# Optimization experiments

Measured on AMD Instinct MI355X. Metric: run time of the kernel, lower is better.

Reference implementation:

```python
import jax, jax.numpy as jnp
import numpy as np

EMBED_DIM = 1024
HEADS = 16
HEAD_DIM = EMBED_DIM // HEADS
DIST_LAMBDA = -0.1
LN_EPS = 1e-5


def setup_inputs() -> dict:
    key = jax.random.key(0)
    ks = jax.random.split(key, 16)
    B, N, D = 32, 4096, EMBED_DIM
    s = 1.0 / np.sqrt(D)
    inp = {
        "query": jax.random.normal(ks[0], (B, D), jnp.float32),
        "context": jax.random.normal(ks[1], (B, N, D), jnp.float32),
        "dist_matrix": jax.random.uniform(ks[2], (B, 1, N), jnp.float32),
        "context_mask": jax.random.randint(ks[3], (B, N), 0, 2, jnp.int32),
        "Wq": jax.random.normal(ks[4], (D, D), jnp.float32) * s,
        "bq": jnp.zeros((D,), jnp.float32),
        "Wk": jax.random.normal(ks[5], (D, D), jnp.float32) * s,
        "bk": jnp.zeros((D,), jnp.float32),
        "Wv": jax.random.normal(ks[6], (D, D), jnp.float32) * s,
        "bv": jnp.zeros((D,), jnp.float32),
        "Wo": jax.random.normal(ks[7], (D, D), jnp.float32) * s,
        "bo": jnp.zeros((D,), jnp.float32),
        "ln_gamma": jnp.ones((D,), jnp.float32),
        "ln_beta": jnp.zeros((D,), jnp.float32),
    }
    return inp


def reference(query, context, dist_matrix, context_mask,
              Wq, bq, Wk, bk, Wv, bv, Wo, bo, ln_gamma, ln_beta):
    B, N, D = context.shape
    H, hd = HEADS, HEAD_DIM
    # projections
    q = (query @ Wq + bq).reshape(B, H, hd)            # [B,H,hd] (single query)
    k = (context @ Wk + bk).reshape(B, N, H, hd)       # [B,N,H,hd]
    v = (context @ Wv + bv).reshape(B, N, H, hd)
    # scores: [B,H,N]
    scores = jnp.einsum("bhd,bnhd->bhn", q, k) / np.sqrt(hd)
    # additive Manhattan-distance bias, broadcast over heads
    scores = scores + dist_matrix * DIST_LAMBDA        # dist_matrix [B,1,N]
    # mask
    scores = jnp.where(context_mask[:, None, :] == 0, -1e9, scores)
    attn = jax.nn.softmax(scores, axis=-1)             # [B,H,N]
    attn_out = jnp.einsum("bhn,bnhd->bhd", attn, v).reshape(B, D)
    output = attn_out @ Wo + bo
    x = query + output
    # LayerNorm
    mu = jnp.mean(x, axis=-1, keepdims=True)
    var = jnp.mean((x - mu) ** 2, axis=-1, keepdims=True)
    return (x - mu) * jax.lax.rsqrt(var + LN_EPS) * ln_gamma + ln_beta
```

## Files before the change

### kernel.cpp

```cpp
#include <hip/hip_runtime.h>
#include <hip/hip_bf16.h>
#include <math.h>

#define DDIM 1024
#define NH 16
#define HDIM 64
#define SCALE 0.125f
#define DLAM -0.1f
#define LNEPS 1e-5f
#define NS 16
#define CHW 16
#define BROW 256
#define CBSTR 1032

typedef short bf16x8 __attribute__((ext_vector_type(8)));
typedef float f32x4 __attribute__((ext_vector_type(4)));

__device__ inline unsigned short f2bf(float x) {
    return __builtin_bit_cast(unsigned short, __float2bfloat16(x));
}
__device__ inline float bfhi2f(unsigned u) {
    return __builtin_bit_cast(float, u & 0xffff0000u);
}
__device__ inline float bflo2f(unsigned u) {
    return __builtin_bit_cast(float, u << 16);
}

__global__ __launch_bounds__(512) void k_q(const float* __restrict__ query,
                                           const float* __restrict__ Wq,
                                           const float* __restrict__ bq,
                                           float* __restrict__ qout) {
    int b = blockIdx.x, c0 = blockIdx.y * 128;
    __shared__ float qs[DDIM];
    __shared__ float ps[512];
    int t = threadIdx.x;
    for (int i = t; i < DDIM; i += 512) qs[i] = query[b * DDIM + i];
    __syncthreads();
    int cl = t & 127;
    int col = c0 + cl;
    int d0 = (t >> 7) * 256;
    float acc = 0.f;
#pragma unroll 8
    for (int d = d0; d < d0 + 256; ++d)
        acc = fmaf(qs[d], Wq[(size_t)d * DDIM + col], acc);
    ps[t] = acc;
    __syncthreads();
    if (t < 128)
        qout[b * DDIM + col] = ps[t] + ps[t + 128] + ps[t + 256] + ps[t + 384] + bq[col];
}

__global__ __launch_bounds__(256) void k_qp(const float* __restrict__ qin,
                                            const float* __restrict__ Wk,
                                            unsigned short* __restrict__ qpb) {
    int b = blockIdx.x, dt = blockIdx.y;
    __shared__ float qs[DDIM];
    for (int i = threadIdx.x; i < DDIM; i += 256) qs[i] = qin[b * DDIM + i];
    __syncthreads();
    int h = threadIdx.x & 15, dl = threadIdx.x >> 4;
    int d = dt * 16 + dl;
    const float* wr = Wk + (size_t)d * DDIM + h * HDIM;
    const float* qh = qs + h * HDIM;
    float acc = 0.f;
#pragma unroll
    for (int j = 0; j < HDIM; ++j) acc = fmaf(wr[j], qh[j], acc);
    qpb[((size_t)(b * NH + h)) * DDIM + d] = f2bf(acc * SCALE);
}

__global__ __launch_bounds__(512) void k_sb(const float* __restrict__ qin,
                                            const float* __restrict__ bk,
                                            float* __restrict__ sb) {
    int idx = threadIdx.x;
    int b = idx >> 4, h = idx & 15;
    float acc = 0.f;
#pragma unroll
    for (int j = 0; j < HDIM; ++j)
        acc = fmaf(bk[h * HDIM + j], qin[b * DDIM + h * HDIM + j], acc);
    sb[idx] = acc * SCALE;
}

__global__ __launch_bounds__(256, 2) void k_flash2(
    const float* __restrict__ ctx, const unsigned short* __restrict__ qpb,
    const float* __restrict__ sb, const float* __restrict__ dist,
    const int* __restrict__ mask, float* __restrict__ partA,
    float* __restrict__ partM, float* __restrict__ partL, int N) {
    __shared__ unsigned short cbuf[2][CHW][CBSTR];
    __shared__ float red[4][CHW][17];
    __shared__ float P_lds[CHW][20];
    __shared__ float fh_lds[NH];
    __shared__ float dls[BROW];

    int b = blockIdx.x, ns = blockIdx.y;
    int t = threadIdx.x, lane = t & 63, w = t >> 6;
    int m = lane & 15, g = lane >> 4;
    int nb0 = ns * BROW;
    int NIT = BROW / CHW;

    {
        float dv = dist[(size_t)b * N + nb0 + t] * DLAM;
        dls[t] = mask[(size_t)b * N + nb0 + t] ? dv : -1e30f;
    }
    bf16x8 qf[8];
#pragma unroll
    for (int j = 0; j < 8; ++j)
        qf[j] = *reinterpret_cast<const bf16x8*>(
            qpb + ((size_t)(b * NH + m)) * DDIM + w * 256 + j * 32 + g * 8);
    float sbv = sb[b * NH + m];

    f32x4 acc[NH];
#pragma unroll
    for (int h = 0; h < NH; ++h) acc[h] = (f32x4){0.f, 0.f, 0.f, 0.f};
    float m_run = -1e30f, l_run = 0.f;

    const float4* cb4 = reinterpret_cast<const float4*>(ctx) +
                        ((size_t)b * N + nb0) * (DDIM / 4);
    float4 inflight[16];

#define LOADC(c)                                               \
    {                                                          \
        const float4* src = cb4 + (size_t)(c) * CHW * (DDIM / 4); \
        _Pragma("unroll") for (int i = 0; i < 16; ++i)         \
            inflight[i] = src[i * 256 + t];                    \
    }
#define WRITECB(buf)                                                        \
    {                                                                       \
        _Pragma("unroll") for (int i = 0; i < 16; ++i) {                    \
            float4 v = inflight[i];                                         \
            unsigned lo = (unsigned)f2bf(v.x) | ((unsigned)f2bf(v.y) << 16);\
            unsigned hi = (unsigned)f2bf(v.z) | ((unsigned)f2bf(v.w) << 16);\
            *reinterpret_cast<uint2*>(&cbuf[buf][i][t * 4]) =               \
                make_uint2(lo, hi);                                         \
        }                                                                   \
    }

    LOADC(0);
    WRITECB(0);
    LOADC(1);

    for (int c = 0; c < NIT; ++c) {
        __syncthreads();
        int buf = c & 1;
        f32x4 cS = {0.f, 0.f, 0.f, 0.f};
#pragma unroll
        for (int j = 0; j < 8; ++j) {
            bf16x8 a = *reinterpret_cast<const bf16x8*>(
                &cbuf[buf][m][w * 256 + j * 32 + g * 8]);
            cS = __builtin_amdgcn_mfma_f32_16x16x32_bf16(a, qf[j], cS, 0, 0, 0);
        }
#pragma unroll
        for (int r = 0; r < 4; ++r) red[w][g * 4 + r][m] = cS[r];
        __syncthreads();
        float S[4];
#pragma unroll
        for (int r = 0; r < 4; ++r) {
            int n = g * 4 + r;
            S[r] = red[0][n][m] + red[1][n][m] + red[2][n][m] + red[3][n][m] +
                   sbv + dls[c * CHW + n];
        }
        float cm = fmaxf(fmaxf(S[0], S[1]), fmaxf(S[2], S[3]));
        cm = fmaxf(cm, __shfl_xor(cm, 16, 64));
        cm = fmaxf(cm, __shfl_xor(cm, 32, 64));
        float mnew = fmaxf(m_run, cm);
        float f = __expf(m_run - mnew);
        float p[4];
        float ls = 0.f;
#pragma unroll
        for (int r = 0; r < 4; ++r) {
            p[r] = __expf(S[r] - mnew);
            ls += p[r];
        }
        ls += __shfl_xor(ls, 16, 64);
        ls += __shfl_xor(ls, 32, 64);
        l_run = l_run * f + ls;
        m_run = mnew;
#pragma unroll
        for (int r = 0; r < 4; ++r) P_lds[g * 4 + r][m] = p[r];
        if (w == 0 && g == 0) fh_lds[m] = f;
        __syncthreads();
#pragma unroll
        for (int h = 0; h < NH; ++h) acc[h] *= fh_lds[h];
        int dq = w * 256 + lane * 4;
#pragma unroll 4
        for (int n = 0; n < CHW; ++n) {
            uint2 cw = *reinterpret_cast<const uint2*>(&cbuf[buf][n][dq]);
            float cv0 = bflo2f(cw.x), cv1 = bfhi2f(cw.x);
            float cv2 = bflo2f(cw.y), cv3 = bfhi2f(cw.y);
            float4 P0 = *reinterpret_cast<const float4*>(&P_lds[n][0]);
            float4 P1 = *reinterpret_cast<const float4*>(&P_lds[n][4]);
            float4 P2 = *reinterpret_cast<const float4*>(&P_lds[n][8]);
            float4 P3 = *reinterpret_cast<const float4*>(&P_lds[n][12]);
            float Pv[16] = {P0.x, P0.y, P0.z, P0.w, P1.x, P1.y, P1.z, P1.w,
                            P2.x, P2.y, P2.z, P2.w, P3.x, P3.y, P3.z, P3.w};
#pragma unroll
            for (int h = 0; h < NH; ++h) {
                acc[h][0] = fmaf(Pv[h], cv0, acc[h][0]);
                acc[h][1] = fmaf(Pv[h], cv1, acc[h][1]);
                acc[h][2] = fmaf(Pv[h], cv2, acc[h][2]);
                acc[h][3] = fmaf(Pv[h], cv3, acc[h][3]);
            }
        }
        __syncthreads();
        if (c + 1 < NIT) {
            WRITECB(buf ^ 1);
            if (c + 2 < NIT) LOADC(c + 2);
        }
    }

    int dq = w * 256 + lane * 4;
#pragma unroll
    for (int h = 0; h < NH; ++h) {
        float4 o = make_float4(acc[h][0], acc[h][1], acc[h][2], acc[h][3]);
        *reinterpret_cast<float4*>(
            partA + ((size_t)((b * NS + ns) * NH + h)) * DDIM + dq) = o;
    }
    if (t < NH) {
        partM[(b * NS + ns) * NH + t] = m_run;
        partL[(b * NS + ns) * NH + t] = l_run;
    }
#undef LOADC
#undef WRITECB
}

__global__ __launch_bounds__(256) void k_comb(const float* __restrict__ partA,
                                              const float* __restrict__ partM,
                                              const float* __restrict__ partL,
                                              float* __restrict__ ctxa) {
    int row = blockIdx.x;
    int b = row >> 4, h = row & 15;
    float M = -1e30f;
#pragma unroll
    for (int ns = 0; ns < NS; ++ns)
        M = fmaxf(M, partM[(b * NS + ns) * NH + h]);
    float denom = 0.f;
#pragma unroll
    for (int ns = 0; ns < NS; ++ns)
        denom = fmaf(__expf(partM[(b * NS + ns) * NH + h] - M),
                     partL[(b * NS + ns) * NH + h], denom);
    float inv = 1.f / denom;
    int d4 = threadIdx.x * 4;
    float4 a = make_float4(0.f, 0.f, 0.f, 0.f);
#pragma unroll 8
    for (int ns = 0; ns < NS; ++ns) {
        float wv = __expf(partM[(b * NS + ns) * NH + h] - M);
        float4 v = *reinterpret_cast<const float4*>(
            partA + ((size_t)((b * NS + ns) * NH + h)) * DDIM + d4);
        a.x = fmaf(wv, v.x, a.x);
        a.y = fmaf(wv, v.y, a.y);
        a.z = fmaf(wv, v.z, a.z);
        a.w = fmaf(wv, v.w, a.w);
    }
    float4 o = make_float4(a.x * inv, a.y * inv, a.z * inv, a.w * inv);
    *reinterpret_cast<float4*>(ctxa + (size_t)row * DDIM + d4) = o;
}

__global__ __launch_bounds__(256) void k_vproj(const float* __restrict__ ctxa,
                                               const float* __restrict__ Wv,
                                               const float* __restrict__ bv,
                                               float* __restrict__ oattn) {
    int b = blockIdx.x, c0 = blockIdx.y * 128;
    int h0 = c0 >> 6;
    __shared__ float cs[2][DDIM];
    __shared__ float ps[256];
    for (int i = threadIdx.x; i < 2 * DDIM; i += 256)
        cs[i >> 10][i & 1023] =
            ctxa[((size_t)(b * NH + h0 + (i >> 10))) * DDIM + (i & 1023)];
    __syncthreads();
    int t = threadIdx.x;
    int cl = t & 127;
    int col = c0 + cl;
    int hl = cl >> 6;
    int d0 = (t >> 7) * 512;
    float acc = 0.f;
#pragma unroll 8
    for (int d = d0; d < d0 + 512; ++d)
        acc = fmaf(cs[hl][d], Wv[(size_t)d * DDIM + col], acc);
    ps[t] = acc;
    __syncthreads();
    if (t < 128) oattn[b * DDIM + col] = ps[t] + ps[t + 128] + bv[col];
}

__global__ __launch_bounds__(256) void k_oproj(const float* __restrict__ query,
                                               const float* __restrict__ oattn,
                                               const float* __restrict__ Wo,
                                               const float* __restrict__ bo,
                                               float* __restrict__ x) {
    int b = blockIdx.x, c0 = blockIdx.y * 128;
    __shared__ float os[DDIM];
    __shared__ float ps[256];
    for (int i = threadIdx.x; i < DDIM; i += 256) os[i] = oattn[b * DDIM + i];
    __syncthreads();
    int t = threadIdx.x;
    int col = c0 + (t & 127);
    int d0 = (t >> 7) * 512;
    float acc = 0.f;
#pragma unroll 8
    for (int d = d0; d < d0 + 512; ++d)
        acc = fmaf(os[d], Wo[(size_t)d * DDIM + col], acc);
    ps[t] = acc;
    __syncthreads();
    if (t < 128)
        x[b * DDIM + col] = query[b * DDIM + col] + ps[t] + ps[t + 128] + bo[col];
}

__global__ __launch_bounds__(256) void k_ln(const float* __restrict__ x,
                                            const float* __restrict__ gamma,
                                            const float* __restrict__ beta,
                                            float* __restrict__ out) {
    int b = blockIdx.x;
    int t = threadIdx.x;
    __shared__ float red[8];
    float xv[4];
    float lsum = 0.f;
#pragma unroll
    for (int k = 0; k < 4; ++k) {
        xv[k] = x[b * DDIM + t + k * 256];
        lsum += xv[k];
    }
#pragma unroll
    for (int off = 32; off > 0; off >>= 1) lsum += __shfl_xor(lsum, off, 64);
    if ((t & 63) == 0) red[t >> 6] = lsum;
    __syncthreads();
    float mu = (red[0] + red[1] + red[2] + red[3]) * (1.f / DDIM);
    float lsq = 0.f;
#pragma unroll
    for (int k = 0; k < 4; ++k) {
        float dx = xv[k] - mu;
        lsq += dx * dx;
    }
#pragma unroll
    for (int off = 32; off > 0; off >>= 1) lsq += __shfl_xor(lsq, off, 64);
    if ((t & 63) == 0) red[4 + (t >> 6)] = lsq;
    __syncthreads();
    float var = (red[4] + red[5] + red[6] + red[7]) * (1.f / DDIM);
    float rstd = rsqrtf(var + LNEPS);
#pragma unroll
    for (int k = 0; k < 4; ++k) {
        int c = t + k * 256;
        out[b * DDIM + c] = (xv[k] - mu) * rstd * gamma[c] + beta[c];
    }
}

extern "C" void kernel_launch(void* const* d_in, const int* in_sizes, int n_in,
                              void* d_out, int out_size, void* d_ws, size_t ws_size,
                              hipStream_t stream) {
    const float* query = (const float*)d_in[0];
    const float* ctx   = (const float*)d_in[1];
    const float* dist  = (const float*)d_in[2];
    const int*   mask  = (const int*)d_in[3];
    const float* Wq = (const float*)d_in[4];
    const float* bq = (const float*)d_in[5];
    const float* Wk = (const float*)d_in[6];
    const float* bk = (const float*)d_in[7];
    const float* Wv = (const float*)d_in[8];
    const float* bv = (const float*)d_in[9];
    const float* Wo = (const float*)d_in[10];
    const float* bo = (const float*)d_in[11];
    const float* gamma = (const float*)d_in[12];
    const float* beta  = (const float*)d_in[13];
    float* out = (float*)d_out;

    int B = in_sizes[0] / DDIM;
    int N = in_sizes[1] / (B * DDIM);

    float* ws = (float*)d_ws;
    float* q = ws;
    unsigned short* qpb = (unsigned short*)(q + (size_t)B * DDIM);
    float* sb = (float*)(qpb + (size_t)B * NH * DDIM);
    float* partA = sb + (size_t)B * NH;
    float* partM = partA + (size_t)B * NS * NH * DDIM;
    float* partL = partM + (size_t)B * NS * NH;
    float* ctxa = partL + (size_t)B * NS * NH;
    float* oattn = ctxa + (size_t)B * NH * DDIM;
    float* xbuf = oattn + (size_t)B * DDIM;

    k_q<<<dim3(B, 8), 512, 0, stream>>>(query, Wq, bq, q);
    k_qp<<<dim3(B, DDIM / 16), 256, 0, stream>>>(q, Wk, qpb);
    k_sb<<<1, B * NH, 0, stream>>>(q, bk, sb);
    k_flash2<<<dim3(B, NS), 256, 0, stream>>>(ctx, qpb, sb, dist, mask,
                                              partA, partM, partL, N);
    k_comb<<<B * NH, 256, 0, stream>>>(partA, partM, partL, ctxa);
    k_vproj<<<dim3(B, 8), 256, 0, stream>>>(ctxa, Wv, bv, oattn);
    k_oproj<<<dim3(B, 8), 256, 0, stream>>>(query, oattn, Wo, bo, xbuf);
    k_ln<<<B, 256, 0, stream>>>(xbuf, gamma, beta, out);
}
```

Measured before the change: 244.7 us.

## Widen flash kernel to 512 threads, single LDS buffer, batch k_qp over 8 queries

The flash-attention stage now runs 512 threads per block across 8 waves. Each wave handles 128 of the feature dimensions with 4 MFMAs, and each thread holds 2 output columns instead of 4, which cuts registers so 4 blocks can target each CU. The double-buffered LDS context tile becomes a single buffer to save LDS, at the cost of serialising the LDS write of the next chunk behind compute. Separately, k_qp now processes 8 batch rows per block so each Wk row is reused across 8 queries instead of being re-read per batch.

```diff
diff --git a/kernel.cpp b/kernel.cpp
--- a/kernel.cpp
+++ b/kernel.cpp
@@ -52,18 +52,26 @@
 __global__ __launch_bounds__(256) void k_qp(const float* __restrict__ qin,
                                             const float* __restrict__ Wk,
                                             unsigned short* __restrict__ qpb) {
-    int b = blockIdx.x, dt = blockIdx.y;
-    __shared__ float qs[DDIM];
-    for (int i = threadIdx.x; i < DDIM; i += 256) qs[i] = qin[b * DDIM + i];
+    int dt = blockIdx.x, bg = blockIdx.y;
+    __shared__ float qs[8][DDIM];
+    for (int i = threadIdx.x; i < 8 * DDIM; i += 256)
+        qs[i >> 10][i & 1023] =
+            qin[(size_t)(bg * 8 + (i >> 10)) * DDIM + (i & 1023)];
     __syncthreads();
     int h = threadIdx.x & 15, dl = threadIdx.x >> 4;
     int d = dt * 16 + dl;
     const float* wr = Wk + (size_t)d * DDIM + h * HDIM;
-    const float* qh = qs + h * HDIM;
-    float acc = 0.f;
-#pragma unroll
-    for (int j = 0; j < HDIM; ++j) acc = fmaf(wr[j], qh[j], acc);
-    qpb[((size_t)(b * NH + h)) * DDIM + d] = f2bf(acc * SCALE);
+    float acc[8] = {0.f, 0.f, 0.f, 0.f, 0.f, 0.f, 0.f, 0.f};
+#pragma unroll
+    for (int j = 0; j < HDIM; ++j) {
+        float wv = wr[j];
+#pragma unroll
+        for (int bb = 0; bb < 8; ++bb)
+            acc[bb] = fmaf(wv, qs[bb][h * HDIM + j], acc[bb]);
+    }
+#pragma unroll
+    for (int bb = 0; bb < 8; ++bb)
+        qpb[((size_t)((bg * 8 + bb) * NH + h)) * DDIM + d] = f2bf(acc[bb] * SCALE);
 }
 
 __global__ __launch_bounds__(512) void k_sb(const float* __restrict__ qin,
@@ -78,13 +86,13 @@
     sb[idx] = acc * SCALE;
 }
 
-__global__ __launch_bounds__(256, 2) void k_flash2(
+__global__ __launch_bounds__(512, 4) void k_flash2(
     const float* __restrict__ ctx, const unsigned short* __restrict__ qpb,
     const float* __restrict__ sb, const float* __restrict__ dist,
     const int* __restrict__ mask, float* __restrict__ partA,
     float* __restrict__ partM, float* __restrict__ partL, int N) {
-    __shared__ unsigned short cbuf[2][CHW][CBSTR];
-    __shared__ float red[4][CHW][17];
+    __shared__ unsigned short cbuf[CHW][CBSTR];
+    __shared__ float red[8][CHW][17];
     __shared__ float P_lds[CHW][20];
     __shared__ float fh_lds[NH];
     __shared__ float dls[BROW];
@@ -93,57 +101,59 @@
     int t = threadIdx.x, lane = t & 63, w = t >> 6;
     int m = lane & 15, g = lane >> 4;
     int nb0 = ns * BROW;
-    int NIT = BROW / CHW;
-
-    {
+    const int NIT = BROW / CHW;
+
+    if (t < BROW) {
         float dv = dist[(size_t)b * N + nb0 + t] * DLAM;
         dls[t] = mask[(size_t)b * N + nb0 + t] ? dv : -1e30f;
     }
-    bf16x8 qf[8];
-#pragma unroll
-    for (int j = 0; j < 8; ++j)
+    bf16x8 qf[4];
+#pragma unroll
+    for (int j = 0; j < 4; ++j)
         qf[j] = *reinterpret_cast<const bf16x8*>(
-            qpb + ((size_t)(b * NH + m)) * DDIM + w * 256 + j * 32 + g * 8);
+            qpb + ((size_t)(b * NH + m)) * DDIM + w * 128 + j * 32 + g * 8);
     float sbv = sb[b * NH + m];
 
-    f32x4 acc[NH];
-#pragma unroll
-    for (int h = 0; h < NH; ++h) acc[h] = (f32x4){0.f, 0.f, 0.f, 0.f};
-    float m_run = -1e30f, l_run = 0.f;
+    float2 acc[NH];
+#pragma unroll
+    for (int h = 0; h < NH; ++h) acc[h] = make_float2(0.f, 0.f);
+    float m_run = -1e20f, l_run = 0.f;
 
     const float4* cb4 = reinterpret_cast<const float4*>(ctx) +
                         ((size_t)b * N + nb0) * (DDIM / 4);
-    float4 inflight[16];
-
-#define LOADC(c)                                               \
-    {                                                          \
+    float4 inflight[8];
+
+#define LOADC(c)                                                  \
+    {                                                             \
         const float4* src = cb4 + (size_t)(c) * CHW * (DDIM / 4); \
-        _Pragma("unroll") for (int i = 0; i < 16; ++i)         \
-            inflight[i] = src[i * 256 + t];                    \
-    }
-#define WRITECB(buf)                                                        \
-    {                                                                       \
-        _Pragma("unroll") for (int i = 0; i < 16; ++i) {                    \
-            float4 v = inflight[i];                                         \
-            unsigned lo = (unsigned)f2bf(v.x) | ((unsigned)f2bf(v.y) << 16);\
-            unsigned hi = (unsigned)f2bf(v.z) | ((unsigned)f2bf(v.w) << 16);\
-            *reinterpret_cast<uint2*>(&cbuf[buf][i][t * 4]) =               \
-                make_uint2(lo, hi);                                         \
-        }                                                                   \
+        _Pragma("unroll") for (int i = 0; i < 8; ++i)             \
+            inflight[i] = src[i * 512 + t];                       \
+    }
+#define WRITECB()                                                            \
+    {                                                                        \
+        _Pragma("unroll") for (int i = 0; i < 8; ++i) {                      \
+            float4 v = inflight[i];                                          \
+            unsigned lo = (unsigned)f2bf(v.x) | ((unsigned)f2bf(v.y) << 16); \
+            unsigned hi = (unsigned)f2bf(v.z) | ((unsigned)f2bf(v.w) << 16); \
+            int row = (i * 512 + t) >> 8;                                    \
+            int c4 = t & 255;                                                \
+            *reinterpret_cast<uint2*>(&cbuf[row][c4 * 4]) =                  \
+                make_uint2(lo, hi);                                          \
+        }                                                                    \
     }
 
     LOADC(0);
-    WRITECB(0);
+    WRITECB();
     LOADC(1);
 
+    int dp = t * 2;
     for (int c = 0; c < NIT; ++c) {
         __syncthreads();
-        int buf = c & 1;
         f32x4 cS = {0.f, 0.f, 0.f, 0.f};
 #pragma unroll
-        for (int j = 0; j < 8; ++j) {
+        for (int j = 0; j < 4; ++j) {
             bf16x8 a = *reinterpret_cast<const bf16x8*>(
-                &cbuf[buf][m][w * 256 + j * 32 + g * 8]);
+                &cbuf[m][w * 128 + j * 32 + g * 8]);
             cS = __builtin_amdgcn_mfma_f32_16x16x32_bf16(a, qf[j], cS, 0, 0, 0);
         }
 #pragma unroll
@@ -153,8 +163,10 @@
 #pragma unroll
         for (int r = 0; r < 4; ++r) {
             int n = g * 4 + r;
-            S[r] = red[0][n][m] + red[1][n][m] + red[2][n][m] + red[3][n][m] +
-                   sbv + dls[c * CHW + n];
+            float s = sbv + dls[c * CHW + n];
+#pragma unroll
+            for (int ww = 0; ww < 8; ++ww) s += red[ww][n][m];
+            S[r] = s;
         }
         float cm = fmaxf(fmaxf(S[0], S[1]), fmaxf(S[2], S[3]));
         cm = fmaxf(cm, __shfl_xor(cm, 16, 64));
@@ -177,13 +189,15 @@
         if (w == 0 && g == 0) fh_lds[m] = f;
         __syncthreads();
 #pragma unroll
-        for (int h = 0; h < NH; ++h) acc[h] *= fh_lds[h];
-        int dq = w * 256 + lane * 4;
+        for (int h = 0; h < NH; ++h) {
+            float fh = fh_lds[h];
+            acc[h].x *= fh;
+            acc[h].y *= fh;
+        }
 #pragma unroll 4
         for (int n = 0; n < CHW; ++n) {
-            uint2 cw = *reinterpret_cast<const uint2*>(&cbuf[buf][n][dq]);
-            float cv0 = bflo2f(cw.x), cv1 = bfhi2f(cw.x);
-            float cv2 = bflo2f(cw.y), cv3 = bfhi2f(cw.y);
+            unsigned cw = *reinterpret_cast<const unsigned*>(&cbuf[n][dp]);
+            float cv0 = bflo2f(cw), cv1 = bfhi2f(cw);
             float4 P0 = *reinterpret_cast<const float4*>(&P_lds[n][0]);
             float4 P1 = *reinterpret_cast<const float4*>(&P_lds[n][4]);
             float4 P2 = *reinterpret_cast<const float4*>(&P_lds[n][8]);
@@ -192,26 +206,21 @@
                             P2.x, P2.y, P2.z, P2.w, P3.x, P3.y, P3.z, P3.w};
 #pragma unroll
             for (int h = 0; h < NH; ++h) {
-                acc[h][0] = fmaf(Pv[h], cv0, acc[h][0]);
-                acc[h][1] = fmaf(Pv[h], cv1, acc[h][1]);
-                acc[h][2] = fmaf(Pv[h], cv2, acc[h][2]);
-                acc[h][3] = fmaf(Pv[h], cv3, acc[h][3]);
+                acc[h].x = fmaf(Pv[h], cv0, acc[h].x);
+                acc[h].y = fmaf(Pv[h], cv1, acc[h].y);
             }
         }
         __syncthreads();
         if (c + 1 < NIT) {
-            WRITECB(buf ^ 1);
+            WRITECB();
             if (c + 2 < NIT) LOADC(c + 2);
         }
     }
 
-    int dq = w * 256 + lane * 4;
-#pragma unroll
-    for (int h = 0; h < NH; ++h) {
-        float4 o = make_float4(acc[h][0], acc[h][1], acc[h][2], acc[h][3]);
-        *reinterpret_cast<float4*>(
-            partA + ((size_t)((b * NS + ns) * NH + h)) * DDIM + dq) = o;
-    }
+#pragma unroll
+    for (int h = 0; h < NH; ++h)
+        *reinterpret_cast<float2*>(
+            partA + ((size_t)((b * NS + ns) * NH + h)) * DDIM + dp) = acc[h];
     if (t < NH) {
         partM[(b * NS + ns) * NH + t] = m_run;
         partL[(b * NS + ns) * NH + t] = l_run;
@@ -373,9 +382,9 @@
     float* xbuf = oattn + (size_t)B * DDIM;
 
     k_q<<<dim3(B, 8), 512, 0, stream>>>(query, Wq, bq, q);
-    k_qp<<<dim3(B, DDIM / 16), 256, 0, stream>>>(q, Wk, qpb);
+    k_qp<<<dim3(DDIM / 16, B / 8), 256, 0, stream>>>(q, Wk, qpb);
     k_sb<<<1, B * NH, 0, stream>>>(q, bk, sb);
-    k_flash2<<<dim3(B, NS), 256, 0, stream>>>(ctx, qpb, sb, dist, mask,
+    k_flash2<<<dim3(B, NS), 512, 0, stream>>>(ctx, qpb, sb, dist, mask,
                                               partA, partM, partL, N);
     k_comb<<<B * NH, 256, 0, stream>>>(partA, partM, partL, ctxa);
     k_vproj<<<dim3(B, 8), 256, 0, stream>>>(ctxa, Wv, bv, oattn);
```

Measured after the change: 279.7 us. 1.14x slower.

## Batch Wk reuse across 8 queries in k_qp and drop a barrier in flash loop

Applied to the files above, without the earlier changes.

k_qp now processes 8 batch rows per block, so each Wk element read from global memory is reused for 8 accumulators instead of being re-read for every batch. This cuts Wk traffic by a factor of eight. In k_flash2 the next-chunk conversion write and prefetch load now sit at the start of each iteration, right after the first barrier, which removes the trailing __syncthreads. The LDS write then overlaps with compute on the other buffer. The k_qp change relies on B being a multiple of 8 and uses 32KB of LDS per block.

```diff
diff --git a/kernel.cpp b/kernel.cpp
--- a/kernel.cpp
+++ b/kernel.cpp
@@ -52,18 +52,26 @@
 __global__ __launch_bounds__(256) void k_qp(const float* __restrict__ qin,
                                             const float* __restrict__ Wk,
                                             unsigned short* __restrict__ qpb) {
-    int b = blockIdx.x, dt = blockIdx.y;
-    __shared__ float qs[DDIM];
-    for (int i = threadIdx.x; i < DDIM; i += 256) qs[i] = qin[b * DDIM + i];
+    int dt = blockIdx.x, bg = blockIdx.y;
+    __shared__ float qs[8][DDIM];
+    for (int i = threadIdx.x; i < 8 * DDIM; i += 256)
+        qs[i >> 10][i & 1023] =
+            qin[(size_t)(bg * 8 + (i >> 10)) * DDIM + (i & 1023)];
     __syncthreads();
     int h = threadIdx.x & 15, dl = threadIdx.x >> 4;
     int d = dt * 16 + dl;
     const float* wr = Wk + (size_t)d * DDIM + h * HDIM;
-    const float* qh = qs + h * HDIM;
-    float acc = 0.f;
-#pragma unroll
-    for (int j = 0; j < HDIM; ++j) acc = fmaf(wr[j], qh[j], acc);
-    qpb[((size_t)(b * NH + h)) * DDIM + d] = f2bf(acc * SCALE);
+    float acc[8] = {0.f, 0.f, 0.f, 0.f, 0.f, 0.f, 0.f, 0.f};
+#pragma unroll
+    for (int j = 0; j < HDIM; ++j) {
+        float wv = wr[j];
+#pragma unroll
+        for (int bb = 0; bb < 8; ++bb)
+            acc[bb] = fmaf(wv, qs[bb][h * HDIM + j], acc[bb]);
+    }
+#pragma unroll
+    for (int bb = 0; bb < 8; ++bb)
+        qpb[((size_t)((bg * 8 + bb) * NH + h)) * DDIM + d] = f2bf(acc[bb] * SCALE);
 }
 
 __global__ __launch_bounds__(512) void k_sb(const float* __restrict__ qin,
@@ -93,7 +101,7 @@
     int t = threadIdx.x, lane = t & 63, w = t >> 6;
     int m = lane & 15, g = lane >> 4;
     int nb0 = ns * BROW;
-    int NIT = BROW / CHW;
+    const int NIT = BROW / CHW;
 
     {
         float dv = dist[(size_t)b * N + nb0 + t] * DLAM;
@@ -115,30 +123,35 @@
                         ((size_t)b * N + nb0) * (DDIM / 4);
     float4 inflight[16];
 
-#define LOADC(c)                                               \
-    {                                                          \
+#define LOADC(c)                                                  \
+    {                                                             \
         const float4* src = cb4 + (size_t)(c) * CHW * (DDIM / 4); \
-        _Pragma("unroll") for (int i = 0; i < 16; ++i)         \
-            inflight[i] = src[i * 256 + t];                    \
-    }
-#define WRITECB(buf)                                                        \
-    {                                                                       \
-        _Pragma("unroll") for (int i = 0; i < 16; ++i) {                    \
-            float4 v = inflight[i];                                         \
-            unsigned lo = (unsigned)f2bf(v.x) | ((unsigned)f2bf(v.y) << 16);\
-            unsigned hi = (unsigned)f2bf(v.z) | ((unsigned)f2bf(v.w) << 16);\
-            *reinterpret_cast<uint2*>(&cbuf[buf][i][t * 4]) =               \
-                make_uint2(lo, hi);                                         \
-        }                                                                   \
+        _Pragma("unroll") for (int i = 0; i < 16; ++i)            \
+            inflight[i] = src[i * 256 + t];                       \
+    }
+#define WRITECB(buf)                                                         \
+    {                                                                        \
+        _Pragma("unroll") for (int i = 0; i < 16; ++i) {                     \
+            float4 v = inflight[i];                                          \
+            unsigned lo = (unsigned)f2bf(v.x) | ((unsigned)f2bf(v.y) << 16); \
+            unsigned hi = (unsigned)f2bf(v.z) | ((unsigned)f2bf(v.w) << 16); \
+            *reinterpret_cast<uint2*>(&cbuf[buf][i][t * 4]) =                \
+                make_uint2(lo, hi);                                          \
+        }                                                                    \
     }
 
     LOADC(0);
     WRITECB(0);
     LOADC(1);
 
+    int dq = w * 256 + lane * 4;
     for (int c = 0; c < NIT; ++c) {
         __syncthreads();
         int buf = c & 1;
+        if (c + 1 < NIT) {
+            WRITECB(buf ^ 1);
+            if (c + 2 < NIT) LOADC(c + 2);
+        }
         f32x4 cS = {0.f, 0.f, 0.f, 0.f};
 #pragma unroll
         for (int j = 0; j < 8; ++j) {
@@ -178,7 +191,6 @@
         __syncthreads();
 #pragma unroll
         for (int h = 0; h < NH; ++h) acc[h] *= fh_lds[h];
-        int dq = w * 256 + lane * 4;
 #pragma unroll 4
         for (int n = 0; n < CHW; ++n) {
             uint2 cw = *reinterpret_cast<const uint2*>(&cbuf[buf][n][dq]);
@@ -198,14 +210,8 @@
                 acc[h][3] = fmaf(Pv[h], cv3, acc[h][3]);
             }
         }
-        __syncthreads();
-        if (c + 1 < NIT) {
-            WRITECB(buf ^ 1);
-            if (c + 2 < NIT) LOADC(c + 2);
-        }
-    }
-
-    int dq = w * 256 + lane * 4;
+    }
+
 #pragma unroll
     for (int h = 0; h < NH; ++h) {
         float4 o = make_float4(acc[h][0], acc[h][1], acc[h][2], acc[h][3]);
@@ -373,7 +379,7 @@
     float* xbuf = oattn + (size_t)B * DDIM;
 
     k_q<<<dim3(B, 8), 512, 0, stream>>>(query, Wq, bq, q);
-    k_qp<<<dim3(B, DDIM / 16), 256, 0, stream>>>(q, Wk, qpb);
+    k_qp<<<dim3(DDIM / 16, B / 8), 256, 0, stream>>>(q, Wk, qpb);
     k_sb<<<1, B * NH, 0, stream>>>(q, bk, sb);
     k_flash2<<<dim3(B, NS), 256, 0, stream>>>(ctx, qpb, sb, dist, mask,
                                               partA, partM, partL, N);
```

Measured after the change: 242.8 us. No clear change (-0.8%).
